# Optimization experiments

Hardware: AMD Instinct MI355X
Metric: run time of the kernel (lower is better)

## Reference

```python
import jax, jax.numpy as jnp
import numpy as np

B = 1024        # number of graphs in batch
NNODES = 64     # nodes per graph
NODE = 4        # node feature size
EDGEF = 2       # edge feature size
HID = 32        # hidden_dim
NFACT = 3       # num_factories
NE = 1024       # edges per graph (self.edges list length)


def setup_inputs() -> dict:
    key = jax.random.key(0)
    ks = jax.random.split(key, 12)
    rng = np.random.default_rng(1)
    # per-graph edge list (self.edges in the torch module)
    edges = rng.integers(0, NNODES, size=(NE, 2))
    edges_src = jnp.asarray(edges[:, 0], dtype=jnp.int32)   # [NE]
    edges_dst = jnp.asarray(edges[:, 1], dtype=jnp.int32)   # [NE]
    # batched edge_index for EdgeConv: same per-graph edges offset by b*NNODES
    offs = np.arange(B, dtype=np.int64)[:, None] * NNODES   # [B,1]
    ei_src = (edges[:, 0][None, :] + offs).reshape(-1)
    ei_dst = (edges[:, 1][None, :] + offs).reshape(-1)
    edge_index = jnp.asarray(np.stack([ei_src, ei_dst], 0), dtype=jnp.int32)  # [2, B*NE]

    N = B * NNODES
    E = B * NE
    x = jax.random.normal(ks[0], (N, NODE), dtype=jnp.float32)
    edge_attr = jax.random.normal(ks[1], (E, EDGEF), dtype=jnp.float32)
    action = jax.random.uniform(ks[2], (B, NE + NFACT), dtype=jnp.float32)

    s = 0.1
    W1 = jax.random.normal(ks[3], (2 * NODE + EDGEF, HID), dtype=jnp.float32) * s
    b1 = jnp.zeros((HID,), jnp.float32)
    W2 = jax.random.normal(ks[4], (HID, HID), dtype=jnp.float32) * s
    b2 = jnp.zeros((HID,), jnp.float32)
    D = (NODE + HID) * 2 + 1  # 73
    Wl = jax.random.normal(ks[5], (D, HID), dtype=jnp.float32) * s
    bl = jnp.zeros((HID,), jnp.float32)
    Wv = jax.random.normal(ks[6], (HID, 1), dtype=jnp.float32) * s
    bv = jnp.zeros((1,), jnp.float32)

    return {"x": x, "edge_index": edge_index, "edge_attr": edge_attr,
            "action": action, "edges_src": edges_src, "edges_dst": edges_dst,
            "W1": W1, "b1": b1, "W2": W2, "b2": b2,
            "Wl": Wl, "bl": bl, "Wv": Wv, "bv": bv}


def reference(x, edge_index, edge_attr, action, edges_src, edges_dst,
              W1, b1, W2, b2, Wl, bl, Wv, bv):
    N = x.shape[0]
    src = edge_index[0]  # flow='target_to_source': x_i = x[src], aggregate at src
    dst = edge_index[1]
    # EdgeConv message: MLP(cat[x_i, x_j, edge_attr])
    tmp = jnp.concatenate([x[src], x[dst], edge_attr], axis=1)  # [E, 10]
    msg = jax.nn.relu(tmp @ W1 + b1) @ W2 + b2                  # [E, HID]
    x_pp = jax.ops.segment_sum(msg, src, num_segments=N)        # scatter-add
    # concat node feats with conv output, split into graphs
    h = jnp.concatenate([x, x_pp], axis=1).reshape(B, NNODES, NODE + HID)  # [B,NN,36]
    # gather per-edge endpoint features
    ef = jnp.concatenate([h[:, edges_src], h[:, edges_dst]], axis=2)       # [B,NE,72]
    # factory features: last NFACT nodes duplicated
    pf = jnp.concatenate([h[:, -NFACT:], h[:, -NFACT:]], axis=-1)          # [B,NF,72]
    feats = jnp.concatenate([ef, pf], axis=1)                               # [B,NE+NF,72]
    concat = jnp.concatenate([feats, action[..., None]], axis=-1)           # [B,NE+NF,73]
    hidden = jax.nn.relu(concat @ Wl + bl)                                  # [B,NE+NF,HID]
    v = hidden @ Wv + bv                                                    # [B,NE+NF,1]
    return jnp.sum(v, axis=1).squeeze(-1)                                   # [B]
```

## Files before the change

### kernel.cpp

```cpp
#include <hip/hip_runtime.h>

#define NNODES 64
#define HID 32
#define NFACT 3
#define NE 1024
#define NROWS (NE + NFACT)
#define TPB 512
#define STR 36
#define QSTRH 20
#define MAXTILES 128
#define EPT (NE / TPB)

typedef short bf16x8 __attribute__((ext_vector_type(8)));
typedef float f32x4  __attribute__((ext_vector_type(4)));
typedef float f32x16 __attribute__((ext_vector_type(16)));
typedef _Float16 f16x2 __attribute__((ext_vector_type(2)));
typedef _Float16 f16x8 __attribute__((ext_vector_type(8)));

__device__ __forceinline__ unsigned pack_bf2(float lo, float hi) {
    unsigned ul = __builtin_bit_cast(unsigned, lo);
    unsigned uh = __builtin_bit_cast(unsigned, hi);
    ul += 0x7fffu + ((ul >> 16) & 1u);
    uh += 0x7fffu + ((uh >> 16) & 1u);
    return (ul >> 16) | (uh & 0xffff0000u);
}
__device__ __forceinline__ short f2bf(float f) {
    unsigned u = __builtin_bit_cast(unsigned, f);
    u += 0x7fffu + ((u >> 16) & 1u);
    return (short)(u >> 16);
}
__device__ __forceinline__ f16x2 pkrtz(float lo, float hi) {
    return __builtin_bit_cast(f16x2, __builtin_amdgcn_cvt_pkrtz(lo, hi));
}
__device__ __forceinline__ f16x2 packh2_rne(float lo, float hi) {
    f16x2 r; r.x = (_Float16)lo; r.y = (_Float16)hi; return r;
}
__device__ __forceinline__ float dot2acc(f16x2 a, f16x2 b, float c) {
#if __has_builtin(__builtin_amdgcn_fdot2)
    return __builtin_amdgcn_fdot2(a, b, c, false);
#else
    return c + (float)a.x * (float)b.x + (float)a.y * (float)b.y;
#endif
}
__device__ __forceinline__ float4 fma4(float a, float4 w, float4 c) {
    c.x = fmaf(a, w.x, c.x); c.y = fmaf(a, w.y, c.y);
    c.z = fmaf(a, w.z, c.z); c.w = fmaf(a, w.w, c.w);
    return c;
}

__global__ __launch_bounds__(TPB, 6) void critic_fused(
    const float* __restrict__ x,
    const float* __restrict__ edge_attr,
    const float* __restrict__ action,
    const int*   __restrict__ es,
    const int*   __restrict__ ed,
    const float* __restrict__ W1,
    const float* __restrict__ b1,
    const float* __restrict__ W2,
    const float* __restrict__ b2,
    const float* __restrict__ Wl,
    const float* __restrict__ bl,
    const float* __restrict__ Wv,
    const float* __restrict__ bv,
    float* __restrict__ out)
{
    const int b    = blockIdx.x;
    const int tid  = threadIdx.x;
    const int lane = tid & 63;
    const int wv   = tid >> 6;
    const int quad = lane >> 4;
    const int m16  = lane & 15;
    const int kh   = quad * 8;
    const f16x2 z2 = { (_Float16)0.f, (_Float16)0.f };

    __shared__ __align__(16) float4 xs4[NNODES];
    __shared__ __align__(16) float  xpp[NNODES * STR];
    __shared__ __align__(16) float  qp0[NNODES * STR];
    __shared__ __align__(16) float  qp1[NNODES * STR];
    __shared__ __align__(16) float  W1s[10 * HID];
    __shared__ float  b1s[HID];
    __shared__ float  wred[TPB / 64];
    __shared__ int    sdeg[NNODES], soff[NNODES], scnt[NNODES];
    __shared__ int    tns[MAXTILES];
    __shared__ int    pep[MAXTILES * 16];
    __shared__ int    snt;

    unsigned* qh0 = (unsigned*)qp0;
    unsigned* qh1 = (unsigned*)qp1;

    if (tid < NNODES) { xs4[tid] = ((const float4*)x)[b * NNODES + tid]; sdeg[tid] = 0; scnt[tid] = 0; }
    if (tid < 80) ((float4*)W1s)[tid] = ((const float4*)W1)[tid];
    if (tid < HID) b1s[tid] = b1[tid];
    if (tid < MAXTILES) tns[tid] = 0;
#pragma unroll
    for (int i = 0; i < MAXTILES * 16 / TPB; i++) pep[tid + i * TPB] = 0xFFF;
    {
        const float4 z4 = make_float4(0.f, 0.f, 0.f, 0.f);
#pragma unroll 1
        for (int i = tid; i < NNODES * STR / 4; i += TPB) ((float4*)xpp)[i] = z4;
    }

    int ces[EPT], ced[EPT];
#pragma unroll
    for (int i = 0; i < EPT; i++) {
        ces[i] = es[tid + i * TPB];
        ced[i] = ed[tid + i * TPB];
    }
    __syncthreads();

#pragma unroll
    for (int i = 0; i < EPT; i++) atomicAdd(&sdeg[ces[i]], 1);
    {
        const int  n  = lane;
        const int  k0 = (wv & 3) * 8;
        const bool g1 = (wv < 4);
        const int  rb = g1 ? 0 : 4;
        const float4 xv = xs4[n];
        float4 qa, qb;
        if (g1) {
            const float4* b1v = (const float4*)&b1s[k0];
            qa = b1v[0]; qb = b1v[1];
        } else {
            qa = make_float4(0.f, 0.f, 0.f, 0.f); qb = qa;
        }
#pragma unroll 1
        for (int i = 0; i < 4; i++) {
            const float xi = (i == 0) ? xv.x : (i == 1) ? xv.y : (i == 2) ? xv.z : xv.w;
            const float4* wa = (const float4*)&W1s[(rb + i) * HID + k0];
            qa = fma4(xi, wa[0], qa); qb = fma4(xi, wa[1], qb);
        }
        uint4 p;
        p.x = __builtin_bit_cast(unsigned, pkrtz(qa.x, qa.y));
        p.y = __builtin_bit_cast(unsigned, pkrtz(qa.z, qa.w));
        p.z = __builtin_bit_cast(unsigned, pkrtz(qb.x, qb.y));
        p.w = __builtin_bit_cast(unsigned, pkrtz(qb.z, qb.w));
        unsigned* dst = g1 ? qh0 : qh1;
        *(uint4*)&dst[n * QSTRH + (wv & 3) * 4] = p;
    }
    __syncthreads();

    if (tid < NNODES) {
        const int cnt = (sdeg[tid] + 15) >> 4;
        int scan = cnt;
#pragma unroll
        for (int o = 1; o < 64; o <<= 1) {
            const int v = __shfl_up(scan, o);
            if (tid >= o) scan += v;
        }
        const int base = scan - cnt;
        soff[tid] = base;
        if (tid == NNODES - 1) snt = scan;
#pragma unroll 1
        for (int j = 0; j < cnt; j++) tns[base + j] = tid;
    }
    __syncthreads();

#pragma unroll
    for (int i = 0; i < EPT; i++) {
        const int n = ces[i];
        const int idx = atomicAdd(&scnt[n], 1);
        pep[soff[n] * 16 + idx] = (tid + i * TPB) | (ced[i] << 12) | (n << 18);
    }
    __syncthreads();

    {
        const float2* ea2 = (const float2*)edge_attr + (size_t)b * NE;
        const int NW   = TPB / 64;
        const int klo  = (lane >> 5) * 8;
        const int klo2 = klo >> 1;
        const int n32  = lane & 31;

        f16x2 w8p[4], w8q[4], w9p[4], w9q[4];
#pragma unroll
        for (int j = 0; j < 4; j++) {
            w8p[j] = packh2_rne(W1s[8 * HID + klo + 2 * j],      W1s[8 * HID + klo + 2 * j + 1]);
            w8q[j] = packh2_rne(W1s[8 * HID + 16 + klo + 2 * j], W1s[8 * HID + 16 + klo + 2 * j + 1]);
            w9p[j] = packh2_rne(W1s[9 * HID + klo + 2 * j],      W1s[9 * HID + klo + 2 * j + 1]);
            w9q[j] = packh2_rne(W1s[9 * HID + 16 + klo + 2 * j], W1s[9 * HID + 16 + klo + 2 * j + 1]);
        }
        f16x8 hfA, hfB;
#pragma unroll
        for (int j = 0; j < 8; j++) {
            hfA[j] = (_Float16)W2[(klo + j) * HID + n32];
            hfB[j] = (_Float16)W2[(16 + klo + j) * HID + n32];
        }

        const int np = (snt + 1) >> 1;

#pragma unroll 1
        for (int p = wv; p < np; p += NW) {
            const int raw = pep[p * 32 + n32];
            const int tA  = tns[2 * p];
            const int tB  = tns[2 * p + 1];
            const int e    = raw & 0xFFF;
            const bool pad = (e == 0xFFF);
            const int d0   = (raw >> 12) & 63;
            const int nd   = (raw >> 18) & 63;
            const float2 ea = ea2[pad ? 0 : e];

            const uint4 A1 = *(const uint4*)&qh0[nd * QSTRH + klo2];
            const uint4 A2 = *(const uint4*)&qh0[nd * QSTRH + 8 + klo2];
            const uint4 G1 = *(const uint4*)&qh1[d0 * QSTRH + klo2];
            const uint4 G2 = *(const uint4*)&qh1[d0 * QSTRH + 8 + klo2];

            const f16x2 ex2 = pkrtz(ea.x, ea.x);
            const f16x2 ey2 = pkrtz(ea.y, ea.y);
            const unsigned pz = pad ? 0u : 0xFFFFFFFFu;

            uint4 pa4, pb4;
#define MSLOT(dst, au, gu, w8, w9) { \
            f16x2 t = __builtin_bit_cast(f16x2, au) + __builtin_bit_cast(f16x2, gu); \
            t = __builtin_elementwise_fma(ex2, w8, t); \
            t = __builtin_elementwise_fma(ey2, w9, t); \
            t = __builtin_elementwise_max(t, z2); \
            dst = __builtin_bit_cast(unsigned, t) & pz; }
            MSLOT(pa4.x, A1.x, G1.x, w8p[0], w9p[0])
            MSLOT(pa4.y, A1.y, G1.y, w8p[1], w9p[1])
            MSLOT(pa4.z, A1.z, G1.z, w8p[2], w9p[2])
            MSLOT(pa4.w, A1.w, G1.w, w8p[3], w9p[3])
            MSLOT(pb4.x, A2.x, G2.x, w8q[0], w9q[0])
            MSLOT(pb4.y, A2.y, G2.y, w8q[1], w9q[1])
            MSLOT(pb4.z, A2.z, G2.z, w8q[2], w9q[2])
            MSLOT(pb4.w, A2.w, G2.w, w8q[3], w9q[3])
#undef MSLOT
            const f16x8 afA = __builtin_bit_cast(f16x8, pa4);
            const f16x8 afB = __builtin_bit_cast(f16x8, pb4);

            f32x16 c;
#pragma unroll
            for (int j = 0; j < 16; j++) c[j] = 0.0f;
            c = __builtin_amdgcn_mfma_f32_32x32x16_f16(afA, hfA, c, 0, 0, 0);
            c = __builtin_amdgcn_mfma_f32_32x32x16_f16(afB, hfB, c, 0, 0, 0);

            float sA = ((c[0] + c[1]) + (c[2] + c[3])) + ((c[4] + c[5]) + (c[6] + c[7]));
            float sB = ((c[8] + c[9]) + (c[10] + c[11])) + ((c[12] + c[13]) + (c[14] + c[15]));
            sA += __shfl_xor(sA, 32);
            sB += __shfl_xor(sB, 32);
            const int   nst = (lane < 32) ? tA : tB;
            const float sv  = (lane < 32) ? sA : sB;
            atomicAdd(&xpp[nst * STR + n32], sv);
        }
    }
    __syncthreads();

    const bool g1p   = (wv < 4);
    const int  cbase = g1p ? 4 : 40;
    const int  xbase = g1p ? 0 : 36;
    bf16x8 bPa, bPb;
#pragma unroll
    for (int j = 0; j < 8; j++) {
        bPa[j] = f2bf(Wl[(cbase + kh + j) * HID + m16]);
        bPb[j] = f2bf(Wl[(cbase + kh + j) * HID + 16 + m16]);
    }
    float wxa[4], wxb[4];
#pragma unroll
    for (int i = 0; i < 4; i++) {
        wxa[i] = Wl[(xbase + i) * HID + m16];
        wxb[i] = Wl[(xbase + i) * HID + 16 + m16];
    }
    const float bca = g1p ? bl[m16] : 0.f;
    const float bcb = g1p ? bl[16 + m16] : 0.f;
    float b2k[8];
#pragma unroll
    for (int j = 0; j < 8; j++) b2k[j] = b2[kh + j];
    const int   mrow = (wv & 3) * 16 + m16;
    const float dn   = (float)sdeg[mrow];

    {
        const float4* xr = (const float4*)&xpp[mrow * STR + kh];
        float4 x0 = xr[0], x1 = xr[1];
        x0.x = fmaf(dn, b2k[0], x0.x); x0.y = fmaf(dn, b2k[1], x0.y);
        x0.z = fmaf(dn, b2k[2], x0.z); x0.w = fmaf(dn, b2k[3], x0.w);
        x1.x = fmaf(dn, b2k[4], x1.x); x1.y = fmaf(dn, b2k[5], x1.y);
        x1.z = fmaf(dn, b2k[6], x1.z); x1.w = fmaf(dn, b2k[7], x1.w);
        uint4 packed;
        packed.x = pack_bf2(x0.x, x0.y);
        packed.y = pack_bf2(x0.z, x0.w);
        packed.z = pack_bf2(x1.x, x1.y);
        packed.w = pack_bf2(x1.z, x1.w);
        const bf16x8 af = __builtin_bit_cast(bf16x8, packed);

        f32x4 ca, cb;
#pragma unroll
        for (int r = 0; r < 4; r++) {
            const float4 xv = xs4[(wv & 3) * 16 + quad * 4 + r];
            float a0 = bca, a1 = bcb;
#pragma unroll
            for (int i = 0; i < 4; i++) {
                const float xi = (i == 0) ? xv.x : (i == 1) ? xv.y : (i == 2) ? xv.z : xv.w;
                a0 = fmaf(xi, wxa[i], a0);
                a1 = fmaf(xi, wxb[i], a1);
            }
            ca[r] = a0; cb[r] = a1;
        }
        ca = __builtin_amdgcn_mfma_f32_16x16x32_bf16(af, bPa, ca, 0, 0, 0);
        cb = __builtin_amdgcn_mfma_f32_16x16x32_bf16(af, bPb, cb, 0, 0, 0);

        __syncthreads();
        unsigned* dsth = g1p ? qh0 : qh1;
#pragma unroll
        for (int r = 0; r < 4; r++) {
            const int row = (wv & 3) * 16 + quad * 4 + r;
            dsth[row * QSTRH + m16] = __builtin_bit_cast(unsigned, pkrtz(ca[r], cb[r]));
        }
    }
    __syncthreads();

    float vsum = 0.0f;
    {
        const float* actb = action + (size_t)b * NROWS;
        const float bvv = bv[0];
        const float* Wl72 = Wl + 72 * HID;
        f16x2 wlh[16], wvh[16];
#pragma unroll
        for (int j = 0; j < 16; j++) {
            wlh[j] = packh2_rne(Wl72[j], Wl72[j + 16]);
            wvh[j] = packh2_rne(Wv[j],  Wv[j + 16]);
        }

#define CSLOT(j, pu, qu, acc) { \
        f16x2 t = __builtin_bit_cast(f16x2, pu) + __builtin_bit_cast(f16x2, qu); \
        t = __builtin_elementwise_fma(a2, wlh[j], t); \
        t = __builtin_elementwise_max(t, z2); \
        acc = dot2acc(t, wvh[j], acc); }

#pragma unroll 1
        for (int i = 0; i < EPT; i++) {
            const int na = ces[i], nb = ced[i];
            const float a = actb[tid + i * TPB];
            const unsigned* ra = &qh0[na * QSTRH];
            const unsigned* rb = &qh1[nb * QSTRH];
            const uint4 Pa0 = *(const uint4*)&ra[0];
            const uint4 Pa1 = *(const uint4*)&ra[4];
            const uint4 Pa2 = *(const uint4*)&ra[8];
            const uint4 Pa3 = *(const uint4*)&ra[12];
            const uint4 Pb0 = *(const uint4*)&rb[0];
            const uint4 Pb1 = *(const uint4*)&rb[4];
            const uint4 Pb2 = *(const uint4*)&rb[8];
            const uint4 Pb3 = *(const uint4*)&rb[12];
            const f16x2 a2 = pkrtz(a, a);
            float v0 = bvv, v1 = 0.0f;
            CSLOT( 0, Pa0.x, Pb0.x, v0) CSLOT( 1, Pa0.y, Pb0.y, v1)
            CSLOT( 2, Pa0.z, Pb0.z, v0) CSLOT( 3, Pa0.w, Pb0.w, v1)
            CSLOT( 4, Pa1.x, Pb1.x, v0) CSLOT( 5, Pa1.y, Pb1.y, v1)
            CSLOT( 6, Pa1.z, Pb1.z, v0) CSLOT( 7, Pa1.w, Pb1.w, v1)
            CSLOT( 8, Pa2.x, Pb2.x, v0) CSLOT( 9, Pa2.y, Pb2.y, v1)
            CSLOT(10, Pa2.z, Pb2.z, v0) CSLOT(11, Pa2.w, Pb2.w, v1)
            CSLOT(12, Pa3.x, Pb3.x, v0) CSLOT(13, Pa3.y, Pb3.y, v1)
            CSLOT(14, Pa3.z, Pb3.z, v0) CSLOT(15, Pa3.w, Pb3.w, v1)
            vsum += v0 + v1;
        }
        if (tid < NFACT) {
            const int r = NE + tid;
            const int na = NNODES - NFACT + tid;
            const float a = actb[r];
            const unsigned* ra = &qh0[na * QSTRH];
            const unsigned* rb = &qh1[na * QSTRH];
            const uint4 Pa0 = *(const uint4*)&ra[0];
            const uint4 Pa1 = *(const uint4*)&ra[4];
            const uint4 Pa2 = *(const uint4*)&ra[8];
            const uint4 Pa3 = *(const uint4*)&ra[12];
            const uint4 Pb0 = *(const uint4*)&rb[0];
            const uint4 Pb1 = *(const uint4*)&rb[4];
            const uint4 Pb2 = *(const uint4*)&rb[8];
            const uint4 Pb3 = *(const uint4*)&rb[12];
            const f16x2 a2 = pkrtz(a, a);
            float v0 = bvv, v1 = 0.0f;
            CSLOT( 0, Pa0.x, Pb0.x, v0) CSLOT( 1, Pa0.y, Pb0.y, v1)
            CSLOT( 2, Pa0.z, Pb0.z, v0) CSLOT( 3, Pa0.w, Pb0.w, v1)
            CSLOT( 4, Pa1.x, Pb1.x, v0) CSLOT( 5, Pa1.y, Pb1.y, v1)
            CSLOT( 6, Pa1.z, Pb1.z, v0) CSLOT( 7, Pa1.w, Pb1.w, v1)
            CSLOT( 8, Pa2.x, Pb2.x, v0) CSLOT( 9, Pa2.y, Pb2.y, v1)
            CSLOT(10, Pa2.z, Pb2.z, v0) CSLOT(11, Pa2.w, Pb2.w, v1)
            CSLOT(12, Pa3.x, Pb3.x, v0) CSLOT(13, Pa3.y, Pb3.y, v1)
            CSLOT(14, Pa3.z, Pb3.z, v0) CSLOT(15, Pa3.w, Pb3.w, v1)
            vsum += v0 + v1;
        }
#undef CSLOT
    }

#pragma unroll
    for (int off = 32; off > 0; off >>= 1)
        vsum += __shfl_down(vsum, off, 64);
    if ((tid & 63) == 0) wred[tid >> 6] = vsum;
    __syncthreads();
    if (tid == 0) {
        float t = 0.0f;
#pragma unroll
        for (int w = 0; w < TPB / 64; w++) t += wred[w];
        out[b] = t;
    }
}

extern "C" void kernel_launch(void* const* d_in, const int* in_sizes, int n_in,
                              void* d_out, int out_size, void* d_ws, size_t ws_size,
                              hipStream_t stream) {
    const float* x         = (const float*)d_in[0];
    const float* edge_attr = (const float*)d_in[2];
    const float* action    = (const float*)d_in[3];
    const int*   es        = (const int*)d_in[4];
    const int*   ed        = (const int*)d_in[5];
    const float* W1        = (const float*)d_in[6];
    const float* b1        = (const float*)d_in[7];
    const float* W2        = (const float*)d_in[8];
    const float* b2        = (const float*)d_in[9];
    const float* Wl        = (const float*)d_in[10];
    const float* bl        = (const float*)d_in[11];
    const float* Wv        = (const float*)d_in[12];
    const float* bv        = (const float*)d_in[13];
    float* out = (float*)d_out;

    critic_fused<<<dim3(out_size), dim3(TPB), 0, stream>>>(
        x, edge_attr, action, es, ed, W1, b1, W2, b2, Wl, bl, Wv, bv, out);
}
```

Before: 122.0 us.

## Build shared edge CSR once in a prologue kernel and prefetch tiles

Moves the per-block degree count, scan and edge bucketing into a single-block prologue kernel that writes the CSR tables to workspace, and the main kernel reads them from global memory. The main kernel also stages edge attributes into shared memory with a coalesced load and software-prefetches the next tile's packed edge entry. This removes redundant atomics and barriers that every block repeated for the identical edge list, but adds a second launch with a serial dependency and global reads in place of LDS reads.

Result: no change. 120.4 us (-1.4%).

```diff
diff --git a/kernel.cpp b/kernel.cpp
--- a/kernel.cpp
+++ b/kernel.cpp
@@ -46,6 +46,53 @@
     c.x = fmaf(a, w.x, c.x); c.y = fmaf(a, w.y, c.y);
     c.z = fmaf(a, w.z, c.z); c.w = fmaf(a, w.w, c.w);
     return c;
+}
+
+__global__ __launch_bounds__(256) void csr_build(
+    const int* __restrict__ es, const int* __restrict__ ed, int* __restrict__ gws)
+{
+    const int tid = threadIdx.x;
+    __shared__ int sdeg[NNODES], soff[NNODES], scnt[NNODES];
+    __shared__ int tns[MAXTILES], snt;
+    __shared__ int pep[MAXTILES * 16];
+    if (tid < NNODES) { sdeg[tid] = 0; scnt[tid] = 0; }
+    if (tid < MAXTILES) tns[tid] = 0;
+#pragma unroll
+    for (int i = tid; i < MAXTILES * 16; i += 256) pep[i] = 0xFFF;
+    int ces[4], ced[4];
+#pragma unroll
+    for (int i = 0; i < 4; i++) { ces[i] = es[tid + i * 256]; ced[i] = ed[tid + i * 256]; }
+    __syncthreads();
+#pragma unroll
+    for (int i = 0; i < 4; i++) atomicAdd(&sdeg[ces[i]], 1);
+    __syncthreads();
+    if (tid < NNODES) {
+        const int cnt = (sdeg[tid] + 15) >> 4;
+        int scan = cnt;
+#pragma unroll
+        for (int o = 1; o < 64; o <<= 1) {
+            const int v = __shfl_up(scan, o);
+            if (tid >= o) scan += v;
+        }
+        const int base = scan - cnt;
+        soff[tid] = base;
+        if (tid == NNODES - 1) snt = scan;
+#pragma unroll 1
+        for (int j = 0; j < cnt; j++) tns[base + j] = tid;
+    }
+    __syncthreads();
+#pragma unroll
+    for (int i = 0; i < 4; i++) {
+        const int n = ces[i];
+        const int idx = atomicAdd(&scnt[n], 1);
+        pep[soff[n] * 16 + idx] = (tid + i * 256) | (ced[i] << 12) | (n << 18);
+    }
+    __syncthreads();
+    if (tid < NNODES) { gws[tid] = sdeg[tid]; gws[64 + tid] = soff[tid]; }
+    if (tid == 0) gws[128] = snt;
+    if (tid < MAXTILES) gws[256 + tid] = tns[tid];
+#pragma unroll
+    for (int i = tid; i < MAXTILES * 16; i += 256) gws[512 + i] = pep[i];
 }
 
 __global__ __launch_bounds__(TPB, 6) void critic_fused(
@@ -62,6 +109,7 @@
     const float* __restrict__ bl,
     const float* __restrict__ Wv,
     const float* __restrict__ bv,
+    const int*   __restrict__ gws,
     float* __restrict__ out)
 {
     const int b    = blockIdx.x;
@@ -78,22 +126,17 @@
     __shared__ __align__(16) float  qp0[NNODES * STR];
     __shared__ __align__(16) float  qp1[NNODES * STR];
     __shared__ __align__(16) float  W1s[10 * HID];
+    __shared__ __align__(16) float  eas[NE * 2];
     __shared__ float  b1s[HID];
     __shared__ float  wred[TPB / 64];
-    __shared__ int    sdeg[NNODES], soff[NNODES], scnt[NNODES];
-    __shared__ int    tns[MAXTILES];
-    __shared__ int    pep[MAXTILES * 16];
-    __shared__ int    snt;
 
     unsigned* qh0 = (unsigned*)qp0;
     unsigned* qh1 = (unsigned*)qp1;
 
-    if (tid < NNODES) { xs4[tid] = ((const float4*)x)[b * NNODES + tid]; sdeg[tid] = 0; scnt[tid] = 0; }
+    if (tid < NNODES) xs4[tid] = ((const float4*)x)[b * NNODES + tid];
     if (tid < 80) ((float4*)W1s)[tid] = ((const float4*)W1)[tid];
     if (tid < HID) b1s[tid] = b1[tid];
-    if (tid < MAXTILES) tns[tid] = 0;
-#pragma unroll
-    for (int i = 0; i < MAXTILES * 16 / TPB; i++) pep[tid + i * TPB] = 0xFFF;
+    ((float4*)eas)[tid] = ((const float4*)edge_attr)[(size_t)b * (NE / 2) + tid];
     {
         const float4 z4 = make_float4(0.f, 0.f, 0.f, 0.f);
 #pragma unroll 1
@@ -108,8 +151,6 @@
     }
     __syncthreads();
 
-#pragma unroll
-    for (int i = 0; i < EPT; i++) atomicAdd(&sdeg[ces[i]], 1);
     {
         const int  n  = lane;
         const int  k0 = (wv & 3) * 8;
@@ -139,32 +180,9 @@
     }
     __syncthreads();
 
-    if (tid < NNODES) {
-        const int cnt = (sdeg[tid] + 15) >> 4;
-        int scan = cnt;
-#pragma unroll
-        for (int o = 1; o < 64; o <<= 1) {
-            const int v = __shfl_up(scan, o);
-            if (tid >= o) scan += v;
-        }
-        const int base = scan - cnt;
-        soff[tid] = base;
-        if (tid == NNODES - 1) snt = scan;
-#pragma unroll 1
-        for (int j = 0; j < cnt; j++) tns[base + j] = tid;
-    }
-    __syncthreads();
-
-#pragma unroll
-    for (int i = 0; i < EPT; i++) {
-        const int n = ces[i];
-        const int idx = atomicAdd(&scnt[n], 1);
-        pep[soff[n] * 16 + idx] = (tid + i * TPB) | (ced[i] << 12) | (n << 18);
-    }
-    __syncthreads();
-
     {
-        const float2* ea2 = (const float2*)edge_attr + (size_t)b * NE;
+        const int* gtns = gws + 256;
+        const int* gpep = gws + 512;
         const int NW   = TPB / 64;
         const int klo  = (lane >> 5) * 8;
         const int klo2 = klo >> 1;
@@ -185,18 +203,29 @@
             hfB[j] = (_Float16)W2[(16 + klo + j) * HID + n32];
         }
 
-        const int np = (snt + 1) >> 1;
-
+        const int np = (gws[128] + 1) >> 1;
+
+        int p = wv;
+        int raw = 0xFFF, tA = 0, tB = 0;
+        if (p < np) {
+            raw = gpep[p * 32 + n32];
+            const int2 tt = *(const int2*)&gtns[2 * p];
+            tA = tt.x; tB = tt.y;
+        }
 #pragma unroll 1
-        for (int p = wv; p < np; p += NW) {
-            const int raw = pep[p * 32 + n32];
-            const int tA  = tns[2 * p];
-            const int tB  = tns[2 * p + 1];
+        while (p < np) {
+            const int pn = p + NW;
+            int rawn = 0xFFF, tAn = 0, tBn = 0;
+            if (pn < np) {
+                rawn = gpep[pn * 32 + n32];
+                const int2 ttn = *(const int2*)&gtns[2 * pn];
+                tAn = ttn.x; tBn = ttn.y;
+            }
             const int e    = raw & 0xFFF;
             const bool pad = (e == 0xFFF);
             const int d0   = (raw >> 12) & 63;
             const int nd   = (raw >> 18) & 63;
-            const float2 ea = ea2[pad ? 0 : e];
+            const float2 ea = *(const float2*)&eas[(pad ? 0 : e) * 2];
 
             const uint4 A1 = *(const uint4*)&qh0[nd * QSTRH + klo2];
             const uint4 A2 = *(const uint4*)&qh0[nd * QSTRH + 8 + klo2];
@@ -239,6 +268,8 @@
             const int   nst = (lane < 32) ? tA : tB;
             const float sv  = (lane < 32) ? sA : sB;
             atomicAdd(&xpp[nst * STR + n32], sv);
+
+            p = pn; raw = rawn; tA = tAn; tB = tBn;
         }
     }
     __syncthreads();
@@ -264,7 +295,7 @@
 #pragma unroll
     for (int j = 0; j < 8; j++) b2k[j] = b2[kh + j];
     const int   mrow = (wv & 3) * 16 + m16;
-    const float dn   = (float)sdeg[mrow];
+    const float dn   = (float)gws[mrow];
 
     {
         const float4* xr = (const float4*)&xpp[mrow * STR + kh];
@@ -409,7 +440,9 @@
     const float* Wv        = (const float*)d_in[12];
     const float* bv        = (const float*)d_in[13];
     float* out = (float*)d_out;
-
+    int*   gws = (int*)d_ws;
+
+    csr_build<<<dim3(1), dim3(256), 0, stream>>>(es, ed, gws);
     critic_fused<<<dim3(out_size), dim3(TPB), 0, stream>>>(
-        x, edge_attr, action, es, ed, W1, b1, W2, b2, Wl, bl, Wv, bv, out);
-}
+        x, edge_attr, action, es, ed, W1, b1, W2, b2, Wl, bl, Wv, bv, gws, out);
+}
```
